# Optimization experiments

Hardware: AMD Instinct MI355X
Metric: run time of the kernel (lower is better)

Reference implementation:

```python
import jax, jax.numpy as jnp
import numpy as np

SQRT_D = 16.0   # sqrt(d), d=256
BETA2 = 18.0    # beta^2 / 2, beta=6
EPS_BN = 1e-5


def _bn1d(x, g, b):
    # eval-mode BatchNorm1d with freshly-initialized running stats (mean=0, var=1)
    scale = g / jnp.sqrt(1.0 + EPS_BN)
    if x.ndim == 3:  # [B, C, N]
        return x * scale[:, None] + b[:, None]
    return x * scale + b  # [B, C]


def _crelu(z):
    return jax.nn.relu(z.real) + 1j * jax.nn.relu(z.imag)


def _sa_layer(x, qk_w, v_w, v_b, t_w, t_b, g, b):
    # x: [B, C, N]; q and k share weights (q_conv.weight = k_conv.weight)
    xq = jnp.einsum('oc,bcn->bno', qk_w, x)            # [B, N, C/4]
    xk = jnp.einsum('oc,bcn->bon', qk_w, x)            # [B, C/4, N]
    xv = jnp.einsum('oc,bcn->bon', v_w, x) + v_b[:, None]
    energy = jnp.einsum('bno,bom->bnm', xq, xk)        # [B, N, N]
    att = jax.nn.softmax(energy, axis=-1)
    att = att / (1e-9 + att.sum(axis=1, keepdims=True))  # sum-normalized over dim=1
    xr = jnp.einsum('bcn,bnm->bcm', xv, att)           # [B, C, N]
    xr = jax.nn.relu(_bn1d(jnp.einsum('oc,bcn->bon', t_w, x - xr) + t_b[:, None], g, b))
    return x + xr


def _forward(x, A, P, cl1_wr, cl1_wi, cl1_br, cl1_bi, cl2_wr, cl2_wi, cl2_br, cl2_bi,
             pt_conv1_w, pt_conv2_w, pt_bn1_g, pt_bn1_b, pt_bn2_g, pt_bn2_b,
             sa_qk_w, sa_v_w, sa_v_b, sa_t_w, sa_t_b, sa_bn_g, sa_bn_b,
             fuse_w, fuse_bn_g, fuse_bn_b, lin1_w, bn6_g, bn6_b,
             lin2_w, lin2_b, bn7_g, bn7_b, lin3_w, lin3_b):
    pts = jnp.transpose(x, (0, 2, 1))                  # [B, N, 3]
    # ---- VecKM: pairwise Gaussian kernel times complex random features ----
    sq = jnp.sum(pts * pts, axis=-1)                   # [B, N]
    D2 = sq[:, :, None] + sq[:, None, :] - 2.0 * jnp.einsum('bnc,bmc->bnm', pts, pts)
    J = jnp.exp(-BETA2 * D2).astype(jnp.complex64)     # [B, N, N]
    eA = jnp.exp(1j * (pts @ A))                       # [B, N, d] complex64
    G = (J @ eA) / eA
    G = G / jnp.linalg.norm(G, axis=-1, keepdims=True) * SQRT_D
    G = G + jnp.exp(1j * (pts @ P))                    # positional encoding
    # ---- ComplexLinear -> ComplexReLU -> ComplexLinear ----
    W1 = (cl1_wr + 1j * cl1_wi).astype(jnp.complex64)
    G = _crelu(G @ W1.T + (cl1_br + 1j * cl1_bi))
    W2 = (cl2_wr + 1j * cl2_wi).astype(jnp.complex64)
    G = G @ W2.T + (cl2_br + 1j * cl2_bi)
    Gr = G.real ** 2 + G.imag ** 2                     # [B, N, 256]
    Gc = jnp.transpose(Gr, (0, 2, 1))                  # [B, 256, N]
    # ---- Point_Transformer_Last ----
    h = jax.nn.relu(_bn1d(jnp.einsum('oc,bcn->bon', pt_conv1_w, Gc), pt_bn1_g, pt_bn1_b))
    h = jax.nn.relu(_bn1d(jnp.einsum('oc,bcn->bon', pt_conv2_w, h), pt_bn2_g, pt_bn2_b))
    feats = []
    for i in range(4):
        h = _sa_layer(h, sa_qk_w[i], sa_v_w[i], sa_v_b[i], sa_t_w[i], sa_t_b[i],
                      sa_bn_g[i], sa_bn_b[i])
        feats.append(h)
    h = jnp.concatenate(feats + [Gc], axis=1)          # [B, 1280, N]
    h = jax.nn.leaky_relu(_bn1d(jnp.einsum('oc,bcn->bon', fuse_w, h), fuse_bn_g, fuse_bn_b), 0.2)
    h = jnp.max(h, axis=-1)                            # adaptive_max_pool1d -> [B, 1024]
    h = jax.nn.leaky_relu(_bn1d(h @ lin1_w.T, bn6_g, bn6_b), 0.2)
    h = jax.nn.leaky_relu(_bn1d(h @ lin2_w.T + lin2_b, bn7_g, bn7_b), 0.2)
    return h @ lin3_w.T + lin3_b                       # [B, 40]


def setup_inputs() -> dict:
    key = jax.random.key(0)
    ks = iter(jax.random.split(key, 64))
    B, N, d = 16, 1024, 256
    r = lambda shape, s=0.05: jax.random.normal(next(ks), shape, dtype=jnp.float32) * s
    inp = {
        'x': jax.random.normal(next(ks), (B, 3, N), dtype=jnp.float32),
        'A': jax.random.normal(next(ks), (3, d), dtype=jnp.float32) * 30.0,
        'P': jax.random.normal(next(ks), (3, d), dtype=jnp.float32),
        'cl1_wr': r((d, d)), 'cl1_wi': r((d, d)), 'cl1_br': r((d,)), 'cl1_bi': r((d,)),
        'cl2_wr': r((d, d)), 'cl2_wi': r((d, d)), 'cl2_br': r((d,)), 'cl2_bi': r((d,)),
        'pt_conv1_w': r((256, 256)), 'pt_conv2_w': r((256, 256)),
        'pt_bn1_g': jnp.ones(256), 'pt_bn1_b': jnp.zeros(256),
        'pt_bn2_g': jnp.ones(256), 'pt_bn2_b': jnp.zeros(256),
        'sa_qk_w': r((4, 64, 256)), 'sa_v_w': r((4, 256, 256)), 'sa_v_b': r((4, 256)),
        'sa_t_w': r((4, 256, 256)), 'sa_t_b': r((4, 256)),
        'sa_bn_g': jnp.ones((4, 256)), 'sa_bn_b': jnp.zeros((4, 256)),
        'fuse_w': r((1024, 1280)), 'fuse_bn_g': jnp.ones(1024), 'fuse_bn_b': jnp.zeros(1024),
        'lin1_w': r((512, 1024)), 'bn6_g': jnp.ones(512), 'bn6_b': jnp.zeros(512),
        'lin2_w': r((256, 512)), 'lin2_b': r((256,)),
        'bn7_g': jnp.ones(256), 'bn7_b': jnp.zeros(256),
        'lin3_w': r((40, 256)), 'lin3_b': r((40,)),
    }
    return inp


def reference(x, A, P, cl1_wr, cl1_wi, cl1_br, cl1_bi, cl2_wr, cl2_wi, cl2_br, cl2_bi,
              pt_conv1_w, pt_conv2_w, pt_bn1_g, pt_bn1_b, pt_bn2_g, pt_bn2_b,
              sa_qk_w, sa_v_w, sa_v_b, sa_t_w, sa_t_b, sa_bn_g, sa_bn_b,
              fuse_w, fuse_bn_g, fuse_bn_b, lin1_w, bn6_g, bn6_b,
              lin2_w, lin2_b, bn7_g, bn7_b, lin3_w, lin3_b):
    return _forward(x, A, P, cl1_wr, cl1_wi, cl1_br, cl1_bi, cl2_wr, cl2_wi, cl2_br, cl2_bi,
                    pt_conv1_w, pt_conv2_w, pt_bn1_g, pt_bn1_b, pt_bn2_g, pt_bn2_b,
                    sa_qk_w, sa_v_w, sa_v_b, sa_t_w, sa_t_b, sa_bn_g, sa_bn_b,
                    fuse_w, fuse_bn_g, fuse_bn_b, lin1_w, bn6_g, bn6_b,
                    lin2_w, lin2_b, bn7_g, bn7_b, lin3_w, lin3_b)
```

## Files before the change

### kernel.cpp

```cpp
#include <hip/hip_runtime.h>
#include <math.h>

#define BB 16
#define NN 1024
#define DD 256

typedef unsigned short u16;
typedef unsigned int uint32;
typedef __attribute__((ext_vector_type(8))) short s8v;
typedef __attribute__((ext_vector_type(4))) float f4v;

__device__ __forceinline__ u16 f2b(float f) {
  uint32 u = __float_as_uint(f);
  return (u16)((u + 0x7fffu + ((u >> 16) & 1u)) >> 16);
}
__device__ __forceinline__ float b2f(u16 u) {
  return __uint_as_float(((uint32)u) << 16);
}
__device__ __forceinline__ float blo(uint32 w) { return __uint_as_float(w << 16); }
__device__ __forceinline__ float bhi(uint32 w) { return __uint_as_float(w & 0xffff0000u); }

__device__ __forceinline__ void gld16(u16* lds, const u16* g) {
  __builtin_amdgcn_global_load_lds(
      (const __attribute__((address_space(1))) unsigned int*)g,
      (__attribute__((address_space(3))) unsigned int*)lds, 16, 0, 0);
}

__device__ __forceinline__ float waveRedSum(float v) {
  #pragma unroll
  for (int o = 32; o; o >>= 1) v += __shfl_xor(v, o, 64);
  return v;
}
__device__ __forceinline__ float waveRedMax(float v) {
  #pragma unroll
  for (int o = 32; o; o >>= 1) v = fmaxf(v, __shfl_xor(v, o, 64));
  return v;
}

__global__ void k_prep(const float* __restrict__ x, float* __restrict__ pts,
                       const float* __restrict__ pt1w, const float* __restrict__ pt2w,
                       const float* __restrict__ qkw, const float* __restrict__ vw,
                       const float* __restrict__ tw, const float* __restrict__ fw,
                       const float* __restrict__ w1r, const float* __restrict__ w1i,
                       const float* __restrict__ w2r, const float* __restrict__ w2i,
                       const float* __restrict__ b1r, const float* __restrict__ b1i,
                       const float* __restrict__ b2r, const float* __restrict__ b2i,
                       u16* __restrict__ wp_pt1, u16* __restrict__ wp_pt2,
                       u16* __restrict__ wp_qkv, u16* __restrict__ wp_t,
                       u16* __restrict__ wp_fuse,
                       u16* __restrict__ W1c, u16* __restrict__ W2c,
                       float* __restrict__ cb1, float* __restrict__ cb2) {
  int i = blockIdx.x * 256 + threadIdx.x;
  if (i < 16384) {
    int b = i >> 10, n = i & 1023;
    const float* xb = x + (size_t)b * 3072;
    pts[i * 3 + 0] = xb[n];
    pts[i * 3 + 1] = xb[1024 + n];
    pts[i * 3 + 2] = xb[2048 + n];
  } else if (i < 81920) {
    int k = i - 16384;  wp_pt1[k] = f2b(pt1w[k]);
  } else if (i < 147456) {
    int k = i - 81920;  wp_pt2[k] = f2b(pt2w[k]);
  } else if (i < 475136) {
    int k = i - 147456;
    int layer = k / 81920, rem = k % 81920;
    int r = rem >> 8, c = rem & 255;
    float v = (r < 64) ? qkw[layer * 16384 + r * 256 + c]
                       : vw[layer * 65536 + (r - 64) * 256 + c];
    wp_qkv[k] = f2b(v);
  } else if (i < 737280) {
    int k = i - 475136; wp_t[k] = f2b(tw[k]);
  } else if (i < 2048000) {
    int k = i - 737280; wp_fuse[k] = f2b(fw[k]);
  } else if (i < 2310144) {
    int k = i - 2048000;
    int op = k >> 9, c2 = k & 511, c = c2 >> 1, pl = c2 & 1;
    float v;
    if (op < 256) v = pl ? -w1i[op * 256 + c] : w1r[op * 256 + c];
    else          v = pl ?  w1r[(op - 256) * 256 + c] : w1i[(op - 256) * 256 + c];
    W1c[k] = f2b(v);
  } else if (i < 2572288) {
    int k = i - 2310144;
    int op = k >> 9, c2 = k & 511, c = c2 >> 1, pl = c2 & 1;
    float v;
    if (op < 256) v = pl ? -w2i[op * 256 + c] : w2r[op * 256 + c];
    else          v = pl ?  w2r[(op - 256) * 256 + c] : w2i[(op - 256) * 256 + c];
    W2c[k] = f2b(v);
  } else if (i < 2572800) {
    int k = i - 2572288; cb1[k] = (k < 256) ? b1r[k] : b1i[k - 256];
  } else if (i < 2573312) {
    int k = i - 2572800; cb2[k] = (k < 256) ? b2r[k] : b2i[k - 256];
  }
}

__global__ void k_phase(const float* __restrict__ pts, const float* __restrict__ A,
                        float2* __restrict__ eA) {
  int i = blockIdx.x * 256 + threadIdx.x;
  int d = i & 255; int bn = i >> 8;
  float p0 = pts[bn * 3], p1 = pts[bn * 3 + 1], p2 = pts[bn * 3 + 2];
  float ta = p0 * A[d] + p1 * A[256 + d] + p2 * A[512 + d];
  float s, c;
  sincosf(ta, &s, &c); eA[i] = make_float2(c, s);
}

__global__ void k_eat(const float2* __restrict__ eA, u16* __restrict__ eAT) {
  int bid = blockIdx.x;
  int dt = bid & 7, nt = (bid >> 3) & 15, b = bid >> 7;
  int d0 = dt * 32, n0 = nt * 64;
  __shared__ u16 cosT[32][72], sinT[32][72];
  int t = threadIdx.x;
  {
    int n = t >> 2, dg = (t & 3) * 8;
    const float2* p = eA + ((size_t)(b * 1024 + n0 + n)) * 256 + d0 + dg;
    #pragma unroll
    for (int j = 0; j < 8; j++) {
      float2 v = p[j];
      cosT[dg + j][n] = f2b(v.x);
      sinT[dg + j][n] = f2b(v.y);
    }
  }
  __syncthreads();
  {
    int rr = t >> 2, ng = (t & 3) * 16;
    int d = rr >> 1, cmp = rr & 1;
    const u16* src = (cmp ? &sinT[d][ng] : &cosT[d][ng]);
    uint4 v0 = *(const uint4*)src;
    uint4 v1 = *(const uint4*)(src + 8);
    u16* dst = eAT + ((size_t)(b * 512 + 2 * d0 + rr)) * 1024 + n0 + ng;
    *(uint4*)dst = v0;
    *(uint4*)(dst + 8) = v1;
  }
}

__global__ void k_jbuild(const float* __restrict__ pts, u16* __restrict__ J) {
  int bid = blockIdx.x;
  int b = bid >> 10, n = bid & 1023;
  int t = threadIdx.x;
  const float* pb = pts + (size_t)b * 3072;
  float pnx = pb[n * 3], pny = pb[n * 3 + 1], pnz = pb[n * 3 + 2];
  int m = t * 4;
  const float* pm = pb + (size_t)m * 3;
  float4 a = *(const float4*)pm;
  float4 bq = *(const float4*)(pm + 4);
  float4 c = *(const float4*)(pm + 8);
  float dx, dy, dz, d2;
  dx = a.x - pnx;  dy = a.y - pny;  dz = a.z - pnz;  d2 = dx*dx + dy*dy + dz*dz;
  float j0 = __expf(-18.0f * d2);
  dx = a.w - pnx;  dy = bq.x - pny; dz = bq.y - pnz; d2 = dx*dx + dy*dy + dz*dz;
  float j1 = __expf(-18.0f * d2);
  dx = bq.z - pnx; dy = bq.w - pny; dz = c.x - pnz;  d2 = dx*dx + dy*dy + dz*dz;
  float j2 = __expf(-18.0f * d2);
  dx = c.y - pnx;  dy = c.z - pny;  dz = c.w - pnz;  d2 = dx*dx + dy*dy + dz*dz;
  float j3 = __expf(-18.0f * d2);
  uint32 lo = (uint32)f2b(j0) | ((uint32)f2b(j1) << 16);
  uint32 hi = (uint32)f2b(j2) | ((uint32)f2b(j3) << 16);
  *(uint2*)(J + (size_t)bid * 1024 + m) = make_uint2(lo, hi);
}

__global__ void k_norm(const float2* __restrict__ M, const float2* __restrict__ eA,
                       const float* __restrict__ pts, const float* __restrict__ P,
                       u16* __restrict__ Gb) {
  int bn = blockIdx.x; int c = threadIdx.x;
  size_t idx = (size_t)bn * DD + c;
  float2 m = M[idx], e = eA[idx];
  float gr = m.x * e.x + m.y * e.y;
  float gi = m.y * e.x - m.x * e.y;
  float s = gr * gr + gi * gi;
  s = waveRedSum(s);
  __shared__ float red[4];
  if ((c & 63) == 0) red[c >> 6] = s;
  __syncthreads();
  float tot = red[0] + red[1] + red[2] + red[3];
  float scale = 16.0f / sqrtf(tot);
  float p0 = pts[bn * 3], p1 = pts[bn * 3 + 1], p2 = pts[bn * 3 + 2];
  float tp = p0 * P[c] + p1 * P[256 + c] + p2 * P[512 + c];
  float sp, cp; sincosf(tp, &sp, &cp);
  uint32 pk = (uint32)f2b(gr * scale + cp) | ((uint32)f2b(gi * scale + sp) << 16);
  *(uint32*)(Gb + idx * 2) = pk;
}

__global__ void k_g2(const u16* __restrict__ G2b, u16* __restrict__ bigT) {
  int i = blockIdx.x * 256 + threadIdx.x;
  int row = i >> 8, c = i & 255;
  float re = b2f(G2b[(size_t)row * 512 + 2 * c]);
  float im = b2f(G2b[(size_t)row * 512 + 2 * c + 1]);
  bigT[(size_t)row * 1280 + 1024 + c] = f2b(re * re + im * im);
}

template<int BM, int STATS, int QKV>
__launch_bounds__(256)
__global__ void k_mm(const u16* __restrict__ Ab, long a_bs, int lda,
                     const u16* __restrict__ Btb, long b_bs, int ldb,
                     int K, int tiles_m, int tiles_n,
                     const float* __restrict__ bias,
                     const float* __restrict__ bng, const float* __restrict__ bnb,
                     const float* __restrict__ cbias,
                     int act,
                     const float* __restrict__ res, long res_bs, int res_sub,
                     float* __restrict__ outF, long outF_bs, int ldF,
                     u16* __restrict__ outB, long outB_bs, int ldBo, int ileave,
                     u16* __restrict__ outT, long outT_bs, int ldT,
                     float* __restrict__ outPool,
                     float* __restrict__ outStats) {
  constexpr int BN = 128;
  constexpr int WM = (BM == 128) ? 64 : 32;
  constexpr int MI = WM / 16;
  __shared__ u16 smem[BN * BM];
  u16* As = smem;
  u16* Bs = smem + BM * 32;
  int t = threadIdx.x;
  int l = t & 63, w = t >> 6;
  int p = l & 15, q = l >> 4;
  int bid = blockIdx.x;
  int tn = bid % tiles_n;
  int tm = (bid / tiles_n) % tiles_m;
  int b  = bid / (tiles_n * tiles_m);
  int m0 = tm * BM, n0 = tn * BN;
  int wm = w >> 1, wn = w & 1;
  const u16* Ap = Ab + (size_t)b * a_bs;
  const u16* Bp = Btb + (size_t)b * b_bs;

  f4v acc[MI][4];
  #pragma unroll
  for (int i = 0; i < MI; i++)
    #pragma unroll
    for (int j = 0; j < 4; j++) acc[i][j] = (f4v){0.f, 0.f, 0.f, 0.f};

  int arow = t >> 2, kg = (t & 3) * 8;
  for (int k0 = 0; k0 < K; k0 += 32) {
    __syncthreads();
    #pragma unroll
    for (int it = 0; it < BM / 64; it++)
      gld16(As + it * 2048 + w * 512,
            Ap + (size_t)(m0 + it * 64 + arow) * lda + k0 + kg);
    #pragma unroll
    for (int it = 0; it < 2; it++)
      gld16(Bs + it * 2048 + w * 512,
            Bp + (size_t)(n0 + it * 64 + arow) * ldb + k0 + kg);
    __syncthreads();
    s8v af[MI], bf[4];
    #pragma unroll
    for (int i = 0; i < MI; i++)
      af[i] = *(const s8v*)&As[(wm * WM + i * 16 + p) * 32 + q * 8];
    #pragma unroll
    for (int j = 0; j < 4; j++)
      bf[j] = *(const s8v*)&Bs[(wn * 64 + j * 16 + p) * 32 + q * 8];
    #pragma unroll
    for (int i = 0; i < MI; i++)
      #pragma unroll
      for (int j = 0; j < 4; j++)
        acc[i][j] = __builtin_amdgcn_mfma_f32_16x16x32_bf16(af[i], bf[j], acc[i][j], 0, 0, 0);
  }

  __syncthreads();

  u16* oB = outB;
  u16* oT = outT;
  if (QKV) { if (tm == 0) oB = nullptr; else oT = nullptr; }

  float cbv[4];
  #pragma unroll
  for (int j = 0; j < 4; j++) {
    int no = n0 + wn * 64 + j * 16 + p;
    cbv[j] = cbias ? cbias[no] : 0.0f;
  }
  float pmax[MI][4];
  #pragma unroll
  for (int i = 0; i < MI; i++)
    #pragma unroll
    for (int r = 0; r < 4; r++) pmax[i][r] = -3.0e38f;
  const float BNS = 0.99999500003749966f;
  #pragma unroll
  for (int i = 0; i < MI; i++) {
    #pragma unroll
    for (int r = 0; r < 4; r++) {
      int mo = m0 + wm * WM + i * 16 + q * 4 + r;
      float mult = 1.f, add = 0.f;
      if (QKV) {
        if (tm > 0 && bias) add = bias[mo - 64];
      } else {
        if (bias) add = bias[mo];
        if (bng) { float s = bng[mo] * BNS; add = add * s + bnb[mo]; mult = s; }
      }
      #pragma unroll
      for (int j = 0; j < 4; j++) {
        int no = n0 + wn * 64 + j * 16 + p;
        float v = acc[i][j][r];
        v = v * mult + add;
        if (cbias) v += cbv[j];
        if (act == 1) v = fmaxf(v, 0.f);
        else if (act == 2) v = v > 0.f ? v : 0.2f * v;
        if (res) {
          float rv = res[(size_t)b * res_bs + (size_t)mo * NN + no];
          v = res_sub ? rv - v : rv + v;
        }
        if (outPool) pmax[i][r] = fmaxf(pmax[i][r], v);
        if (outF) outF[(size_t)b * outF_bs + (size_t)mo * ldF + no] = v;
        if (oB) {
          int moB = QKV ? (mo - 64) : mo;
          int noo = ileave ? (((no & 255) << 1) | (no >> 8)) : no;
          oB[(size_t)b * outB_bs + (size_t)moB * ldBo + noo] = f2b(v);
        }
        if (oT) smem[(wn * 64 + j * 16 + p) * BM + (mo - m0)] = f2b(v);
      }
    }
  }
  if (oT) {
    __syncthreads();
    constexpr int CPR = BM / 8;
    constexpr int RPP = 256 / CPR;
    int row0 = t / CPR, cg = (t % CPR) * 8;
    for (int rr = row0; rr < BN; rr += RPP) {
      float4 v = *(const float4*)&smem[rr * BM + cg];
      *(float4*)(oT + (size_t)b * outT_bs + (size_t)(n0 + rr) * ldT + m0 + cg) = v;
    }
  }
  if (outPool) {
    float* pf = (float*)smem;
    #pragma unroll
    for (int i = 0; i < MI; i++)
      #pragma unroll
      for (int r = 0; r < 4; r++) {
        float m = pmax[i][r];
        #pragma unroll
        for (int o = 1; o < 16; o <<= 1) m = fmaxf(m, __shfl_xor(m, o, 64));
        if (p == 0) pf[(wm * WM + i * 16 + q * 4 + r) * 2 + wn] = m;
      }
    __syncthreads();
    if (t < BM) {
      float mv = fmaxf(pf[t * 2], pf[t * 2 + 1]);
      outPool[((size_t)b * tiles_n + tn) * (size_t)(tiles_m * BM) + m0 + t] = mv;
    }
  }
  if (STATS) {
    float* sm1 = (float*)smem;
    float* sm2 = sm1 + BM * 2;
    #pragma unroll
    for (int i = 0; i < MI; i++)
      #pragma unroll
      for (int r = 0; r < 4; r++) {
        float m = fmaxf(fmaxf(acc[i][0][r], acc[i][1][r]), fmaxf(acc[i][2][r], acc[i][3][r]));
        #pragma unroll
        for (int o = 1; o < 16; o <<= 1) m = fmaxf(m, __shfl_xor(m, o, 64));
        if (p == 0) sm1[(wm * WM + i * 16 + q * 4 + r) * 2 + wn] = m;
      }
    __syncthreads();
    #pragma unroll
    for (int i = 0; i < MI; i++)
      #pragma unroll
      for (int r = 0; r < 4; r++) {
        int row = wm * WM + i * 16 + q * 4 + r;
        float g = fmaxf(sm1[row * 2], sm1[row * 2 + 1]);
        float s = __expf(acc[i][0][r] - g) + __expf(acc[i][1][r] - g) +
                  __expf(acc[i][2][r] - g) + __expf(acc[i][3][r] - g);
        #pragma unroll
        for (int o = 1; o < 16; o <<= 1) s += __shfl_xor(s, o, 64);
        if (p == 0) sm2[row * 2 + wn] = s;
      }
    __syncthreads();
    if (t < BM) {
      float g = fmaxf(sm1[t * 2], sm1[t * 2 + 1]);
      float ssum = sm2[t * 2] + sm2[t * 2 + 1];
      *(float2*)(outStats + (((size_t)b * (tiles_m * BM) + m0 + t) * tiles_n + tn) * 2)
          = make_float2(g, ssum);
    }
  }
}

__launch_bounds__(256)
__global__ void k_xratt(const u16* __restrict__ xv_, const u16* __restrict__ E,
                        const float* __restrict__ part_,
                        const float* __restrict__ XinF, long xinF_bs,
                        u16* __restrict__ diffT) {
  __shared__ u16 smem[16384];
  __shared__ float colred[128][4];
  __shared__ float rmS[1024];
  __shared__ float riS[1024];
  u16* As = smem;
  u16* Bs = smem + 4096;
  int t = threadIdx.x;
  int l = t & 63, w = t >> 6;
  int p = l & 15, q = l >> 4;
  int bid = blockIdx.x;
  int mt = bid & 7, ct = (bid >> 3) & 1, b = bid >> 4;
  int c0 = ct * 128, m0 = mt * 128;
  int wm = w >> 1, wn = w & 1;
  const u16* Ap = xv_ + (size_t)b * 262144;
  const u16* Ep = E + ((size_t)b << 20);
  {
    const float2* pbase = (const float2*)(part_ + (size_t)b * 16384);
    for (int row = t; row < 1024; row += 256) {
      const float2* pp = pbase + row * 8;
      float2 vv[8];
      #pragma unroll
      for (int k = 0; k < 8; k++) vv[k] = pp[k];
      float g = vv[0].x;
      #pragma unroll
      for (int k = 1; k < 8; k++) g = fmaxf(g, vv[k].x);
      float s = 0.f;
      #pragma unroll
      for (int k = 0; k < 8; k++) s += vv[k].y * __expf(vv[k].x - g);
      rmS[row] = g;
      riS[row] = 1.0f / s;
    }
  }
  f4v acc[4][4];
  #pragma unroll
  for (int i = 0; i < 4; i++)
    #pragma unroll
    for (int j = 0; j < 4; j++) acc[i][j] = (f4v){0.f, 0.f, 0.f, 0.f};
  float colpart0 = 0.f, colpart1 = 0.f;
  int arow = t >> 2, kg = (t & 3) * 8;
  for (int k0 = 0; k0 < 1024; k0 += 32) {
    __syncthreads();
    #pragma unroll
    for (int it = 0; it < 2; it++)
      gld16(As + it * 2048 + w * 512,
            Ap + (size_t)(c0 + it * 64 + arow) * 1024 + k0 + kg);
    float4 ma0 = *(const float4*)&rmS[k0 + kg];
    float4 ma1 = *(const float4*)&rmS[k0 + kg + 4];
    float4 ia0 = *(const float4*)&riS[k0 + kg];
    float4 ia1 = *(const float4*)&riS[k0 + kg + 4];
    #pragma unroll
    for (int it = 0; it < 2; it++) {
      int r = it * 64 + arow;
      uint4 e8 = *(const uint4*)(Ep + (size_t)(m0 + r) * 1024 + k0 + kg);
      float p0 = __expf(blo(e8.x) - ma0.x) * ia0.x;
      float p1 = __expf(bhi(e8.x) - ma0.y) * ia0.y;
      float p2 = __expf(blo(e8.y) - ma0.z) * ia0.z;
      float p3 = __expf(bhi(e8.y) - ma0.w) * ia0.w;
      float p4 = __expf(blo(e8.z) - ma1.x) * ia1.x;
      float p5 = __expf(bhi(e8.z) - ma1.y) * ia1.y;
      float p6 = __expf(blo(e8.w) - ma1.z) * ia1.z;
      float p7 = __expf(bhi(e8.w) - ma1.w) * ia1.w;
      float s8 = ((p0 + p1) + (p2 + p3)) + ((p4 + p5) + (p6 + p7));
      if (it == 0) colpart0 += s8; else colpart1 += s8;
      uint32 w0 = (uint32)f2b(p0) | ((uint32)f2b(p1) << 16);
      uint32 w1 = (uint32)f2b(p2) | ((uint32)f2b(p3) << 16);
      uint32 w2 = (uint32)f2b(p4) | ((uint32)f2b(p5) << 16);
      uint32 w3 = (uint32)f2b(p6) | ((uint32)f2b(p7) << 16);
      *(uint4*)&Bs[r * 32 + kg] = make_uint4(w0, w1, w2, w3);
    }
    __syncthreads();
    s8v af[4], bf[4];
    #pragma unroll
    for (int i = 0; i < 4; i++)
      af[i] = *(const s8v*)&As[(wm * 64 + i * 16 + p) * 32 + q * 8];
    #pragma unroll
    for (int j = 0; j < 4; j++)
      bf[j] = *(const s8v*)&Bs[(wn * 64 + j * 16 + p) * 32 + q * 8];
    #pragma unroll
    for (int i = 0; i < 4; i++)
      #pragma unroll
      for (int j = 0; j < 4; j++)
        acc[i][j] = __builtin_amdgcn_mfma_f32_16x16x32_bf16(af[i], bf[j], acc[i][j], 0, 0, 0);
  }
  colred[arow][t & 3] = colpart0;
  colred[64 + arow][t & 3] = colpart1;
  __syncthreads();
  float csv[4];
  #pragma unroll
  for (int j = 0; j < 4; j++) {
    int ml = wn * 64 + j * 16 + p;
    csv[j] = 1.0f / (1e-9f + colred[ml][0] + colred[ml][1] + colred[ml][2] + colred[ml][3]);
  }
  #pragma unroll
  for (int i = 0; i < 4; i++) {
    #pragma unroll
    for (int r = 0; r < 4; r++) {
      int cl = wm * 64 + i * 16 + q * 4 + r;
      int c = c0 + cl;
      #pragma unroll
      for (int j = 0; j < 4; j++) {
        int ml = wn * 64 + j * 16 + p;
        float v = acc[i][j][r] * csv[j];
        float rv = XinF[(size_t)b * xinF_bs + (size_t)c * 1024 + m0 + ml];
        smem[ml * 128 + cl] = f2b(rv - v);
      }
    }
  }
  __syncthreads();
  int rr0 = t >> 4, cg = (t & 15) * 8;
  #pragma unroll
  for (int k = 0; k < 8; k++) {
    int rr = rr0 + k * 16;
    *(float4*)(diffT + (size_t)b * 262144 + (size_t)(m0 + rr) * 256 + c0 + cg) =
        *(const float4*)&smem[rr * 128 + cg];
  }
}

__global__ void k_pool8(const float* __restrict__ pp, float* __restrict__ pool) {
  int i = blockIdx.x * 256 + threadIdx.x;
  int b = i >> 10, o = i & 1023;
  const float* base = pp + (size_t)b * 8192 + o;
  float m = base[0];
  #pragma unroll
  for (int tn = 1; tn < 8; tn++) m = fmaxf(m, base[tn * 1024]);
  pool[i] = m;
}

__global__ void k_fc(const float* __restrict__ in, int Cc,
                     const float* __restrict__ W,
                     const float* __restrict__ bias,
                     const float* __restrict__ bng, const float* __restrict__ bnb,
                     int act, float* __restrict__ out, int O) {
  int i = blockIdx.x * 256 + threadIdx.x;
  if (i >= BB * O) return;
  int b = i / O, o = i % O;
  const float* xp = in + (size_t)b * Cc;
  const float* wp = W + (size_t)o * Cc;
  float s = 0.f;
  for (int c = 0; c < Cc; c += 4) {
    float4 xv = *(const float4*)(xp + c);
    float4 wv = *(const float4*)(wp + c);
    s += xv.x * wv.x + xv.y * wv.y + xv.z * wv.z + xv.w * wv.w;
  }
  if (bias) s += bias[o];
  const float BNS = 0.99999500003749966f;
  if (bng) s = s * (bng[o] * BNS) + bnb[o];
  if (act == 2) s = s > 0.f ? s : 0.2f * s;
  else if (act == 1) s = fmaxf(s, 0.f);
  out[i] = s;
}

extern "C" void kernel_launch(void* const* d_in, const int* in_sizes, int n_in,
                              void* d_out, int out_size, void* d_ws, size_t ws_size,
                              hipStream_t stream) {
  const float* x        = (const float*)d_in[0];
  const float* A        = (const float*)d_in[1];
  const float* P        = (const float*)d_in[2];
  const float* cl1_wr   = (const float*)d_in[3];
  const float* cl1_wi   = (const float*)d_in[4];
  const float* cl1_br   = (const float*)d_in[5];
  const float* cl1_bi   = (const float*)d_in[6];
  const float* cl2_wr   = (const float*)d_in[7];
  const float* cl2_wi   = (const float*)d_in[8];
  const float* cl2_br   = (const float*)d_in[9];
  const float* cl2_bi   = (const float*)d_in[10];
  const float* pt_c1_w  = (const float*)d_in[11];
  const float* pt_c2_w  = (const float*)d_in[12];
  const float* pt_bn1_g = (const float*)d_in[13];
  const float* pt_bn1_b = (const float*)d_in[14];
  const float* pt_bn2_g = (const float*)d_in[15];
  const float* pt_bn2_b = (const float*)d_in[16];
  const float* sa_qk_w  = (const float*)d_in[17];
  const float* sa_v_w   = (const float*)d_in[18];
  const float* sa_v_b   = (const float*)d_in[19];
  const float* sa_t_w   = (const float*)d_in[20];
  const float* sa_t_b   = (const float*)d_in[21];
  const float* sa_bn_g  = (const float*)d_in[22];
  const float* sa_bn_b  = (const float*)d_in[23];
  const float* fuse_w   = (const float*)d_in[24];
  const float* fuse_g   = (const float*)d_in[25];
  const float* fuse_b   = (const float*)d_in[26];
  const float* lin1_w   = (const float*)d_in[27];
  const float* bn6_g    = (const float*)d_in[28];
  const float* bn6_b    = (const float*)d_in[29];
  const float* lin2_w   = (const float*)d_in[30];
  const float* lin2_b   = (const float*)d_in[31];
  const float* bn7_g    = (const float*)d_in[32];
  const float* bn7_b    = (const float*)d_in[33];
  const float* lin3_w   = (const float*)d_in[34];
  const float* lin3_b   = (const float*)d_in[35];

  float* ws = (float*)d_ws;
  const size_t oPts  = 0;
  const size_t oS    = 65536;
  const size_t oBigT = oS + 16777216;
  const size_t oXf0  = oBigT + 10485760;
  const size_t oXf1  = oXf0 + 4194304;
  const size_t oH1T  = oXf1 + 4194304;
  const size_t oH2T  = oH1T + 2097152;
  const size_t oXkT  = oH2T + 2097152;
  const size_t oXv   = oXkT + 524288;
  const size_t oAux  = oXv + 2097152;
  const size_t oGb   = oAux + 8388608;
  const size_t oW1c  = oGb + 4194304;
  const size_t oW2c  = oW1c + 131072;
  const size_t oCb1  = oW2c + 131072;
  const size_t oCb2  = oCb1 + 512;
  const size_t oPool = oCb2 + 512;
  const size_t oFc1  = oPool + 16384;
  const size_t oFc2  = oFc1 + 8192;
  const size_t oWp   = oFc2 + 4096;

  float*  pts  = ws + oPts;
  float2* eA   = (float2*)(ws + oS);
  float2* Mj   = (float2*)(ws + oS + 8388608);
  u16*    G1b  = (u16*)(ws + oS);
  u16*    G2b  = (u16*)(ws + oS + 8388608);
  u16*    Eb   = (u16*)(ws + oS);
  float*  poolP= ws + oS + 8388608;
  u16*    bigT = (u16*)(ws + oBigT);
  float*  Xf0  = ws + oXf0;
  float*  Xf1  = ws + oXf1;
  u16*    h1T  = (u16*)(ws + oH1T);
  u16*    diffT= (u16*)(ws + oH1T);
  u16*    h2T  = (u16*)(ws + oH2T);
  u16*    xkT  = (u16*)(ws + oXkT);
  u16*    xv   = (u16*)(ws + oXv);
  u16*    eAT  = (u16*)(ws + oAux);
  u16*    Jb   = (u16*)(ws + oAux + 4194304);
  float*  partP= ws + oAux;
  u16*    Gb   = (u16*)(ws + oGb);
  u16*    W1c  = (u16*)(ws + oW1c);
  u16*    W2c  = (u16*)(ws + oW2c);
  float*  cb1  = ws + oCb1;
  float*  cb2  = ws + oCb2;
  float*  pool = ws + oPool;
  float*  fc1  = ws + oFc1;
  float*  fc2  = ws + oFc2;
  u16*    wp   = (u16*)(ws + oWp);
  u16* wp_pt1  = wp;
  u16* wp_pt2  = wp + 65536;
  u16* wp_qkv  = wp + 131072;
  u16* wp_t    = wp + 458752;
  u16* wp_fuse = wp + 720896;

  k_prep<<<10052, 256, 0, stream>>>(x, pts,
      pt_c1_w, pt_c2_w, sa_qk_w, sa_v_w, sa_t_w, fuse_w,
      cl1_wr, cl1_wi, cl2_wr, cl2_wi, cl1_br, cl1_bi, cl2_br, cl2_bi,
      wp_pt1, wp_pt2, wp_qkv, wp_t, wp_fuse, W1c, W2c, cb1, cb2);

  k_phase<<<16384, 256, 0, stream>>>(pts, A, eA);
  k_eat<<<2048, 256, 0, stream>>>(eA, eAT);
  k_jbuild<<<16384, 256, 0, stream>>>(pts, Jb);
  k_mm<128,0,0><<<512, 256, 0, stream>>>(Jb, 1048576, 1024, eAT, 524288, 1024, 1024, 8, 4,
      nullptr, nullptr, nullptr, nullptr, 0, nullptr, 0, 0,
      (float*)Mj, 524288, 512, nullptr, 0, 0, 0, nullptr, 0, 0, nullptr, nullptr);
  k_norm<<<BB * NN, 256, 0, stream>>>(Mj, eA, pts, P, Gb);

  k_mm<128,0,0><<<512, 256, 0, stream>>>(Gb, 0, 512, W1c, 0, 512, 512, 128, 4,
      nullptr, nullptr, nullptr, cb1, 1, nullptr, 0, 0,
      nullptr, 0, 0, G1b, 0, 512, 1, nullptr, 0, 0, nullptr, nullptr);
  k_mm<128,0,0><<<512, 256, 0, stream>>>(G1b, 0, 512, W2c, 0, 512, 512, 128, 4,
      nullptr, nullptr, nullptr, cb2, 0, nullptr, 0, 0,
      nullptr, 0, 0, G2b, 0, 512, 1, nullptr, 0, 0, nullptr, nullptr);
  k_g2<<<16384, 256, 0, stream>>>(G2b, bigT);

  const long bsBigT = 1310720;
  const long bsH256 = 262144;
  const long bsXkT  = 65536;
  const long bsXvU  = 262144;
  const long bsF    = 262144;
  const long bsEU   = 1048576;

  k_mm<128,0,0><<<256, 256, 0, stream>>>(wp_pt1, 0, 256, bigT + 1024, bsBigT, 1280, 256, 2, 8,
      nullptr, pt_bn1_g, pt_bn1_b, nullptr, 1, nullptr, 0, 0,
      nullptr, 0, 0, nullptr, 0, 0, 0, h1T, bsH256, 256, nullptr, nullptr);
  k_mm<128,0,0><<<256, 256, 0, stream>>>(wp_pt2, 0, 256, h1T, bsH256, 256, 256, 2, 8,
      nullptr, pt_bn2_g, pt_bn2_b, nullptr, 1, nullptr, 0, 0,
      Xf0, bsF, 1024, nullptr, 0, 0, 0, h2T, bsH256, 256, nullptr, nullptr);

  for (int i = 0; i < 4; i++) {
    const u16* XinT   = (i == 0) ? h2T : (bigT + (i - 1) * 256);
    long       xinT_bs= (i == 0) ? bsH256 : bsBigT;
    int        xinT_ld= (i == 0) ? 256 : 1280;
    float*     XinF   = (i & 1) ? Xf1 : Xf0;
    float*     XoutF  = (i & 1) ? Xf0 : Xf1;
    const u16* qkvw = wp_qkv + (size_t)i * 81920;
    const u16* tw   = wp_t + (size_t)i * 65536;

    k_mm<64,0,1><<<BB * 5 * 8, 256, 0, stream>>>(qkvw, 0, 256, XinT, xinT_bs, xinT_ld, 256, 5, 8,
        sa_v_b + i * 256, nullptr, nullptr, nullptr, 0, nullptr, 0, 0,
        nullptr, 0, 0, xv, bsXvU, 1024, 0, xkT, bsXkT, 64, nullptr, nullptr);
    k_mm<128,1,0><<<1024, 256, 0, stream>>>(xkT, bsXkT, 64, xkT, bsXkT, 64, 64, 8, 8,
        nullptr, nullptr, nullptr, nullptr, 0, nullptr, 0, 0,
        nullptr, 0, 0, Eb, bsEU, 1024, 0, nullptr, 0, 0, nullptr, partP);
    k_xratt<<<256, 256, 0, stream>>>(xv, Eb, partP, XinF, bsF, diffT);
    k_mm<128,0,0><<<256, 256, 0, stream>>>(tw, 0, 256, diffT, bsH256, 256, 256, 2, 8,
        sa_t_b + i * 256, sa_bn_g + i * 256, sa_bn_b + i * 256, nullptr, 1,
        XinF, bsF, 0,
        XoutF, bsF, 1024, nullptr, 0, 0, 0, bigT + i * 256, bsBigT, 1280, nullptr, nullptr);
  }

  k_mm<128,0,0><<<1024, 256, 0, stream>>>(wp_fuse, 0, 1280, bigT, bsBigT, 1280, 1280, 8, 8,
      nullptr, fuse_g, fuse_b, nullptr, 2, nullptr, 0, 0,
      nullptr, 0, 0, nullptr, 0, 0, 0, nullptr, 0, 0, poolP, nullptr);
  k_pool8<<<64, 256, 0, stream>>>(poolP, pool);

  k_fc<<<32, 256, 0, stream>>>(pool, 1024, lin1_w, nullptr, bn6_g, bn6_b, 2, fc1, 512);
  k_fc<<<16, 256, 0, stream>>>(fc1, 512, lin2_w, lin2_b, bn7_g, bn7_b, 2, fc2, 256);
  k_fc<<<3, 256, 0, stream>>>(fc2, 256, lin3_w, lin3_b, nullptr, nullptr, 0, (float*)d_out, 40);
}
```

Measured before the change: 1.015 ms.

## Fuse phase/transpose/J-build kernels, halve xratt tile, merge MLP head

```diff
diff --git a/kernel.cpp b/kernel.cpp
--- a/kernel.cpp
+++ b/kernel.cpp
@@ -29,11 +29,6 @@
 __device__ __forceinline__ float waveRedSum(float v) {
   #pragma unroll
   for (int o = 32; o; o >>= 1) v += __shfl_xor(v, o, 64);
-  return v;
-}
-__device__ __forceinline__ float waveRedMax(float v) {
-  #pragma unroll
-  for (int o = 32; o; o >>= 1) v = fmaxf(v, __shfl_xor(v, o, 64));
   return v;
 }
 
@@ -93,68 +88,65 @@
   }
 }
 
-__global__ void k_phase(const float* __restrict__ pts, const float* __restrict__ A,
-                        float2* __restrict__ eA) {
-  int i = blockIdx.x * 256 + threadIdx.x;
-  int d = i & 255; int bn = i >> 8;
-  float p0 = pts[bn * 3], p1 = pts[bn * 3 + 1], p2 = pts[bn * 3 + 2];
-  float ta = p0 * A[d] + p1 * A[256 + d] + p2 * A[512 + d];
-  float s, c;
-  sincosf(ta, &s, &c); eA[i] = make_float2(c, s);
-}
-
-__global__ void k_eat(const float2* __restrict__ eA, u16* __restrict__ eAT) {
+__global__ void k_pe(const float* __restrict__ pts, const float* __restrict__ A,
+                     float2* __restrict__ eA, u16* __restrict__ eAT,
+                     u16* __restrict__ J) {
+  __shared__ u16 cosT[32][72], sinT[32][72];
   int bid = blockIdx.x;
-  int dt = bid & 7, nt = (bid >> 3) & 15, b = bid >> 7;
-  int d0 = dt * 32, n0 = nt * 64;
-  __shared__ u16 cosT[32][72], sinT[32][72];
   int t = threadIdx.x;
-  {
+  if (bid < 2048) {
+    int dt = bid & 7, nt = (bid >> 3) & 15, b = bid >> 7;
+    int d0 = dt * 32, n0 = nt * 64;
     int n = t >> 2, dg = (t & 3) * 8;
-    const float2* p = eA + ((size_t)(b * 1024 + n0 + n)) * 256 + d0 + dg;
+    const float* pp = pts + ((size_t)(b * 1024 + n0 + n)) * 3;
+    float p0 = pp[0], p1 = pp[1], p2 = pp[2];
+    float2 ev[8];
     #pragma unroll
     for (int j = 0; j < 8; j++) {
-      float2 v = p[j];
-      cosT[dg + j][n] = f2b(v.x);
-      sinT[dg + j][n] = f2b(v.y);
-    }
-  }
-  __syncthreads();
-  {
-    int rr = t >> 2, ng = (t & 3) * 16;
-    int d = rr >> 1, cmp = rr & 1;
-    const u16* src = (cmp ? &sinT[d][ng] : &cosT[d][ng]);
-    uint4 v0 = *(const uint4*)src;
-    uint4 v1 = *(const uint4*)(src + 8);
-    u16* dst = eAT + ((size_t)(b * 512 + 2 * d0 + rr)) * 1024 + n0 + ng;
-    *(uint4*)dst = v0;
-    *(uint4*)(dst + 8) = v1;
-  }
-}
-
-__global__ void k_jbuild(const float* __restrict__ pts, u16* __restrict__ J) {
-  int bid = blockIdx.x;
-  int b = bid >> 10, n = bid & 1023;
-  int t = threadIdx.x;
-  const float* pb = pts + (size_t)b * 3072;
-  float pnx = pb[n * 3], pny = pb[n * 3 + 1], pnz = pb[n * 3 + 2];
-  int m = t * 4;
-  const float* pm = pb + (size_t)m * 3;
-  float4 a = *(const float4*)pm;
-  float4 bq = *(const float4*)(pm + 4);
-  float4 c = *(const float4*)(pm + 8);
-  float dx, dy, dz, d2;
-  dx = a.x - pnx;  dy = a.y - pny;  dz = a.z - pnz;  d2 = dx*dx + dy*dy + dz*dz;
-  float j0 = __expf(-18.0f * d2);
-  dx = a.w - pnx;  dy = bq.x - pny; dz = bq.y - pnz; d2 = dx*dx + dy*dy + dz*dz;
-  float j1 = __expf(-18.0f * d2);
-  dx = bq.z - pnx; dy = bq.w - pny; dz = c.x - pnz;  d2 = dx*dx + dy*dy + dz*dz;
-  float j2 = __expf(-18.0f * d2);
-  dx = c.y - pnx;  dy = c.z - pny;  dz = c.w - pnz;  d2 = dx*dx + dy*dy + dz*dz;
-  float j3 = __expf(-18.0f * d2);
-  uint32 lo = (uint32)f2b(j0) | ((uint32)f2b(j1) << 16);
-  uint32 hi = (uint32)f2b(j2) | ((uint32)f2b(j3) << 16);
-  *(uint2*)(J + (size_t)bid * 1024 + m) = make_uint2(lo, hi);
+      int d = d0 + dg + j;
+      float ta = p0 * A[d] + p1 * A[256 + d] + p2 * A[512 + d];
+      float s, c; sincosf(ta, &s, &c);
+      ev[j] = make_float2(c, s);
+      cosT[dg + j][n] = f2b(c);
+      sinT[dg + j][n] = f2b(s);
+    }
+    float2* dst = eA + ((size_t)(b * 1024 + n0 + n)) * 256 + d0 + dg;
+    #pragma unroll
+    for (int j = 0; j < 8; j++) dst[j] = ev[j];
+    __syncthreads();
+    {
+      int rr = t >> 2, ng = (t & 3) * 16;
+      int d = rr >> 1, cmp = rr & 1;
+      const u16* src = (cmp ? &sinT[d][ng] : &cosT[d][ng]);
+      uint4 v0 = *(const uint4*)src;
+      uint4 v1 = *(const uint4*)(src + 8);
+      u16* dstT = eAT + ((size_t)(b * 512 + 2 * d0 + rr)) * 1024 + n0 + ng;
+      *(uint4*)dstT = v0;
+      *(uint4*)(dstT + 8) = v1;
+    }
+  } else {
+    int bid2 = bid - 2048;
+    int b = bid2 >> 10, n = bid2 & 1023;
+    const float* pb = pts + (size_t)b * 3072;
+    float pnx = pb[n * 3], pny = pb[n * 3 + 1], pnz = pb[n * 3 + 2];
+    int m = t * 4;
+    const float* pm = pb + (size_t)m * 3;
+    float4 a = *(const float4*)pm;
+    float4 bq = *(const float4*)(pm + 4);
+    float4 c = *(const float4*)(pm + 8);
+    float dx, dy, dz, d2;
+    dx = a.x - pnx;  dy = a.y - pny;  dz = a.z - pnz;  d2 = dx*dx + dy*dy + dz*dz;
+    float j0 = __expf(-18.0f * d2);
+    dx = a.w - pnx;  dy = bq.x - pny; dz = bq.y - pnz; d2 = dx*dx + dy*dy + dz*dz;
+    float j1 = __expf(-18.0f * d2);
+    dx = bq.z - pnx; dy = bq.w - pny; dz = c.x - pnz;  d2 = dx*dx + dy*dy + dz*dz;
+    float j2 = __expf(-18.0f * d2);
+    dx = c.y - pnx;  dy = c.z - pny;  dz = c.w - pnz;  d2 = dx*dx + dy*dy + dz*dz;
+    float j3 = __expf(-18.0f * d2);
+    uint32 lo = (uint32)f2b(j0) | ((uint32)f2b(j1) << 16);
+    uint32 hi = (uint32)f2b(j2) | ((uint32)f2b(j3) << 16);
+    *(uint2*)(J + (size_t)bid2 * 1024 + m) = make_uint2(lo, hi);
+  }
 }
 
 __global__ void k_norm(const float2* __restrict__ M, const float2* __restrict__ eA,
@@ -373,7 +365,7 @@
                         const float* __restrict__ XinF, long xinF_bs,
                         u16* __restrict__ diffT) {
   __shared__ u16 smem[16384];
-  __shared__ float colred[128][4];
+  __shared__ float colred[64][4];
   __shared__ float rmS[1024];
   __shared__ float riS[1024];
   u16* As = smem;
@@ -382,9 +374,9 @@
   int l = t & 63, w = t >> 6;
   int p = l & 15, q = l >> 4;
   int bid = blockIdx.x;
-  int mt = bid & 7, ct = (bid >> 3) & 1, b = bid >> 4;
-  int c0 = ct * 128, m0 = mt * 128;
-  int wm = w >> 1, wn = w & 1;
+  int mt = bid & 15, ct = (bid >> 4) & 1, b = bid >> 5;
+  int c0 = ct * 128, m0 = mt * 64;
+  int wm = w;
   const u16* Ap = xv_ + (size_t)b * 262144;
   const u16* Ep = E + ((size_t)b << 20);
   {
@@ -404,12 +396,12 @@
       riS[row] = 1.0f / s;
     }
   }
-  f4v acc[4][4];
-  #pragma unroll
-  for (int i = 0; i < 4; i++)
+  f4v acc[2][4];
+  #pragma unroll
+  for (int i = 0; i < 2; i++)
     #pragma unroll
     for (int j = 0; j < 4; j++) acc[i][j] = (f4v){0.f, 0.f, 0.f, 0.f};
-  float colpart0 = 0.f, colpart1 = 0.f;
+  float colpart = 0.f;
   int arow = t >> 2, kg = (t & 3) * 8;
   for (int k0 = 0; k0 < 1024; k0 += 32) {
     __syncthreads();
@@ -421,9 +413,8 @@
     float4 ma1 = *(const float4*)&rmS[k0 + kg + 4];
     float4 ia0 = *(const float4*)&riS[k0 + kg];
     float4 ia1 = *(const float4*)&riS[k0 + kg + 4];
-    #pragma unroll
-    for (int it = 0; it < 2; it++) {
-      int r = it * 64 + arow;
+    {
+      int r = arow;
       uint4 e8 = *(const uint4*)(Ep + (size_t)(m0 + r) * 1024 + k0 + kg);
       float p0 = __expf(blo(e8.x) - ma0.x) * ia0.x;
       float p1 = __expf(bhi(e8.x) - ma0.y) * ia0.y;
@@ -434,7 +425,7 @@
       float p6 = __expf(blo(e8.w) - ma1.z) * ia1.z;
       float p7 = __expf(bhi(e8.w) - ma1.w) * ia1.w;
       float s8 = ((p0 + p1) + (p2 + p3)) + ((p4 + p5) + (p6 + p7));
-      if (it == 0) colpart0 += s8; else colpart1 += s8;
+      colpart += s8;
       uint32 w0 = (uint32)f2b(p0) | ((uint32)f2b(p1) << 16);
       uint32 w1 = (uint32)f2b(p2) | ((uint32)f2b(p3) << 16);
       uint32 w2 = (uint32)f2b(p4) | ((uint32)f2b(p5) << 16);
@@ -442,85 +433,109 @@
       *(uint4*)&Bs[r * 32 + kg] = make_uint4(w0, w1, w2, w3);
     }
     __syncthreads();
-    s8v af[4], bf[4];
-    #pragma unroll
-    for (int i = 0; i < 4; i++)
-      af[i] = *(const s8v*)&As[(wm * 64 + i * 16 + p) * 32 + q * 8];
+    s8v af[2], bf[4];
+    #pragma unroll
+    for (int i = 0; i < 2; i++)
+      af[i] = *(const s8v*)&As[(wm * 32 + i * 16 + p) * 32 + q * 8];
     #pragma unroll
     for (int j = 0; j < 4; j++)
-      bf[j] = *(const s8v*)&Bs[(wn * 64 + j * 16 + p) * 32 + q * 8];
-    #pragma unroll
-    for (int i = 0; i < 4; i++)
+      bf[j] = *(const s8v*)&Bs[(j * 16 + p) * 32 + q * 8];
+    #pragma unroll
+    for (int i = 0; i < 2; i++)
       #pragma unroll
       for (int j = 0; j < 4; j++)
         acc[i][j] = __builtin_amdgcn_mfma_f32_16x16x32_bf16(af[i], bf[j], acc[i][j], 0, 0, 0);
   }
-  colred[arow][t & 3] = colpart0;
-  colred[64 + arow][t & 3] = colpart1;
+  colred[arow][t & 3] = colpart;
   __syncthreads();
   float csv[4];
   #pragma unroll
   for (int j = 0; j < 4; j++) {
-    int ml = wn * 64 + j * 16 + p;
+    int ml = j * 16 + p;
     csv[j] = 1.0f / (1e-9f + colred[ml][0] + colred[ml][1] + colred[ml][2] + colred[ml][3]);
   }
-  #pragma unroll
-  for (int i = 0; i < 4; i++) {
+  u16* T = smem;
+  #pragma unroll
+  for (int i = 0; i < 2; i++) {
     #pragma unroll
     for (int r = 0; r < 4; r++) {
-      int cl = wm * 64 + i * 16 + q * 4 + r;
+      int cl = wm * 32 + i * 16 + q * 4 + r;
       int c = c0 + cl;
       #pragma unroll
       for (int j = 0; j < 4; j++) {
-        int ml = wn * 64 + j * 16 + p;
+        int ml = j * 16 + p;
         float v = acc[i][j][r] * csv[j];
         float rv = XinF[(size_t)b * xinF_bs + (size_t)c * 1024 + m0 + ml];
-        smem[ml * 128 + cl] = f2b(rv - v);
+        T[ml * 128 + cl] = f2b(rv - v);
       }
     }
   }
   __syncthreads();
   int rr0 = t >> 4, cg = (t & 15) * 8;
   #pragma unroll
-  for (int k = 0; k < 8; k++) {
+  for (int k = 0; k < 4; k++) {
     int rr = rr0 + k * 16;
     *(float4*)(diffT + (size_t)b * 262144 + (size_t)(m0 + rr) * 256 + c0 + cg) =
-        *(const float4*)&smem[rr * 128 + cg];
-  }
-}
-
-__global__ void k_pool8(const float* __restrict__ pp, float* __restrict__ pool) {
-  int i = blockIdx.x * 256 + threadIdx.x;
-  int b = i >> 10, o = i & 1023;
-  const float* base = pp + (size_t)b * 8192 + o;
-  float m = base[0];
-  #pragma unroll
-  for (int tn = 1; tn < 8; tn++) m = fmaxf(m, base[tn * 1024]);
-  pool[i] = m;
-}
-
-__global__ void k_fc(const float* __restrict__ in, int Cc,
-                     const float* __restrict__ W,
-                     const float* __restrict__ bias,
-                     const float* __restrict__ bng, const float* __restrict__ bnb,
-                     int act, float* __restrict__ out, int O) {
-  int i = blockIdx.x * 256 + threadIdx.x;
-  if (i >= BB * O) return;
-  int b = i / O, o = i % O;
-  const float* xp = in + (size_t)b * Cc;
-  const float* wp = W + (size_t)o * Cc;
-  float s = 0.f;
-  for (int c = 0; c < Cc; c += 4) {
-    float4 xv = *(const float4*)(xp + c);
-    float4 wv = *(const float4*)(wp + c);
-    s += xv.x * wv.x + xv.y * wv.y + xv.z * wv.z + xv.w * wv.w;
-  }
-  if (bias) s += bias[o];
+        *(const float4*)&T[rr * 128 + cg];
+  }
+}
+
+__global__ void k_head(const float* __restrict__ poolP,
+                       const float* __restrict__ lin1_w,
+                       const float* __restrict__ bn6_g, const float* __restrict__ bn6_b,
+                       const float* __restrict__ lin2_w, const float* __restrict__ lin2_b,
+                       const float* __restrict__ bn7_g, const float* __restrict__ bn7_b,
+                       const float* __restrict__ lin3_w, const float* __restrict__ lin3_b,
+                       float* __restrict__ out) {
+  int b = blockIdx.x, t = threadIdx.x;
+  __shared__ float pl[1024];
+  __shared__ float h1[512];
+  __shared__ float h2[256];
   const float BNS = 0.99999500003749966f;
-  if (bng) s = s * (bng[o] * BNS) + bnb[o];
-  if (act == 2) s = s > 0.f ? s : 0.2f * s;
-  else if (act == 1) s = fmaxf(s, 0.f);
-  out[i] = s;
+  for (int o = t; o < 1024; o += 256) {
+    const float* base = poolP + (size_t)b * 8192 + o;
+    float m = base[0];
+    #pragma unroll
+    for (int tn = 1; tn < 8; tn++) m = fmaxf(m, base[tn * 1024]);
+    pl[o] = m;
+  }
+  __syncthreads();
+  for (int o = t; o < 512; o += 256) {
+    const float* wp = lin1_w + (size_t)o * 1024;
+    float s = 0.f;
+    for (int c = 0; c < 1024; c += 4) {
+      float4 xv = *(const float4*)(pl + c);
+      float4 wv = *(const float4*)(wp + c);
+      s += xv.x * wv.x + xv.y * wv.y + xv.z * wv.z + xv.w * wv.w;
+    }
+    s = s * (bn6_g[o] * BNS) + bn6_b[o];
+    h1[o] = s > 0.f ? s : 0.2f * s;
+  }
+  __syncthreads();
+  {
+    int o = t;
+    const float* wp = lin2_w + (size_t)o * 512;
+    float s = 0.f;
+    for (int c = 0; c < 512; c += 4) {
+      float4 xv = *(const float4*)(h1 + c);
+      float4 wv = *(const float4*)(wp + c);
+      s += xv.x * wv.x + xv.y * wv.y + xv.z * wv.z + xv.w * wv.w;
+    }
+    s += lin2_b[o];
+    s = s * (bn7_g[o] * BNS) + bn7_b[o];
+    h2[o] = s > 0.f ? s : 0.2f * s;
+  }
+  __syncthreads();
+  if (t < 40) {
+    const float* wp = lin3_w + (size_t)t * 256;
+    float s = 0.f;
+    for (int c = 0; c < 256; c += 4) {
+      float4 xv = *(const float4*)(h2 + c);
+      float4 wv = *(const float4*)(wp + c);
+      s += xv.x * wv.x + xv.y * wv.y + xv.z * wv.z + xv.w * wv.w;
+    }
+    out[b * 40 + t] = s + lin3_b[t];
+  }
 }
 
 extern "C" void kernel_launch(void* const* d_in, const int* in_sizes, int n_in,
@@ -607,9 +622,6 @@
   u16*    W2c  = (u16*)(ws + oW2c);
   float*  cb1  = ws + oCb1;
   float*  cb2  = ws + oCb2;
-  float*  pool = ws + oPool;
-  float*  fc1  = ws + oFc1;
-  float*  fc2  = ws + oFc2;
   u16*    wp   = (u16*)(ws + oWp);
   u16* wp_pt1  = wp;
   u16* wp_pt2  = wp + 65536;
@@ -622,9 +634,7 @@
       cl1_wr, cl1_wi, cl2_wr, cl2_wi, cl1_br, cl1_bi, cl2_br, cl2_bi,
       wp_pt1, wp_pt2, wp_qkv, wp_t, wp_fuse, W1c, W2c, cb1, cb2);
 
-  k_phase<<<16384, 256, 0, stream>>>(pts, A, eA);
-  k_eat<<<2048, 256, 0, stream>>>(eA, eAT);
-  k_jbuild<<<16384, 256, 0, stream>>>(pts, Jb);
+  k_pe<<<18432, 256, 0, stream>>>(pts, A, eA, eAT, Jb);
   k_mm<128,0,0><<<512, 256, 0, stream>>>(Jb, 1048576, 1024, eAT, 524288, 1024, 1024, 8, 4,
       nullptr, nullptr, nullptr, nullptr, 0, nullptr, 0, 0,
       (float*)Mj, 524288, 512, nullptr, 0, 0, 0, nullptr, 0, 0, nullptr, nullptr);
@@ -667,7 +677,7 @@
     k_mm<128,1,0><<<1024, 256, 0, stream>>>(xkT, bsXkT, 64, xkT, bsXkT, 64, 64, 8, 8,
         nullptr, nullptr, nullptr, nullptr, 0, nullptr, 0, 0,
         nullptr, 0, 0, Eb, bsEU, 1024, 0, nullptr, 0, 0, nullptr, partP);
-    k_xratt<<<256, 256, 0, stream>>>(xv, Eb, partP, XinF, bsF, diffT);
+    k_xratt<<<512, 256, 0, stream>>>(xv, Eb, partP, XinF, bsF, diffT);
     k_mm<128,0,0><<<256, 256, 0, stream>>>(tw, 0, 256, diffT, bsH256, 256, 256, 2, 8,
         sa_t_b + i * 256, sa_bn_g + i * 256, sa_bn_b + i * 256, nullptr, 1,
         XinF, bsF, 0,
@@ -677,9 +687,7 @@
   k_mm<128,0,0><<<1024, 256, 0, stream>>>(wp_fuse, 0, 1280, bigT, bsBigT, 1280, 1280, 8, 8,
       nullptr, fuse_g, fuse_b, nullptr, 2, nullptr, 0, 0,
       nullptr, 0, 0, nullptr, 0, 0, 0, nullptr, 0, 0, poolP, nullptr);
-  k_pool8<<<64, 256, 0, stream>>>(poolP, pool);
-
-  k_fc<<<32, 256, 0, stream>>>(pool, 1024, lin1_w, nullptr, bn6_g, bn6_b, 2, fc1, 512);
-  k_fc<<<16, 256, 0, stream>>>(fc1, 512, lin2_w, lin2_b, bn7_g, bn7_b, 2, fc2, 256);
-  k_fc<<<3, 256, 0, stream>>>(fc2, 256, lin3_w, lin3_b, nullptr, nullptr, 0, (float*)d_out, 40);
-}
+
+  k_head<<<16, 256, 0, stream>>>(poolP, lin1_w, bn6_g, bn6_b,
+      lin2_w, lin2_b, bn7_g, bn7_b, lin3_w, lin3_b, (float*)d_out);
+}
```

Result: faster. 988.5 us (-2.6%).
